# Kernel optimization log

Hardware: AMD Instinct MI355X
Metric: run time of the kernel (lower is better)

The kernel has to match this reference:

```python
import jax, jax.numpy as jnp
import numpy as np

B, A, D, F, O, NB = 64, 1024, 5, 256, 256, 6  # batch, max_atoms, max_degree, ishape, oshape, bond feat dim


def setup_inputs() -> dict:
    key = jax.random.key(0)
    k1, k2, k3, k4 = jax.random.split(key, 4)
    atoms = jax.random.normal(k1, (B, A, F), dtype=jnp.float32)
    bonds = jax.random.normal(k2, (B, A, D, NB), dtype=jnp.float32)
    # -1 marks missing neighbor (degree padding); valid indices in [0, A)
    edges = jax.random.randint(k3, (B, A, D), -1, A)
    # xavier-normal-ish init for the 6 degree-specific weights, stacked [6, F+NB, O]
    scale = (2.0 / (F + NB + O)) ** 0.5
    degW = jax.random.normal(k4, (6, F + NB, O), dtype=jnp.float32) * scale
    b = jnp.full((1, O), 0.01, dtype=jnp.float32)
    return {"atoms": atoms, "bonds": bonds, "edges": edges, "degW": degW, "b": b}


def reference(atoms, bonds, edges, degW, b):
    # atoms: [B, A, F]; bonds: [B, A, D, NB]; edges: [B, A, D] int (-1 = pad)
    degrees = (edges != -1).sum(-1, keepdims=True)  # [B, A, 1]
    # pad a zero row at index 0 so edge -1 -> 0 gathers the mask value 0
    padded = jnp.pad(atoms, ((0, 0), (1, 0), (0, 0)))  # [B, A+1, F]
    neigh = jax.vmap(lambda p, e: p[e])(padded, edges + 1)  # [B, A, D, F]
    summed_atom = atoms + neigh.sum(axis=2)  # include_self=True
    feats = jnp.concatenate([summed_atom, bonds.sum(axis=2)], axis=-1)  # [B, A, F+NB]
    out = jnp.zeros((atoms.shape[0], atoms.shape[1], degW.shape[-1]), atoms.dtype)
    for d in range(6):  # fixed small structural loop over degree buckets
        mask = (degrees == d).astype(atoms.dtype)  # [B, A, 1]
        out = out + jax.nn.sigmoid(feats @ degW[d] + b) * mask
    return out
```

## Files before the change

### kernel.cpp

```cpp
#include <hip/hip_runtime.h>
#include <cstdint>

#define BATCH  64
#define NATOMS 1024
#define DEG    5
#define FIN    256
#define OOUT   256
#define NBF    6
#define KDIM   262
#define NKT    9
#define MROWS  (BATCH * NATOMS)
#define MT     32
#define AS     296

#define FRAG_SHORTS (16 * NKT * 64 * 8)

typedef __attribute__((ext_vector_type(8))) short bf16x8;
typedef __attribute__((ext_vector_type(4))) float f32x4;

__device__ __forceinline__ unsigned short f2bf(float x) {
    unsigned u = __float_as_uint(x);
    u += 0x7fff + ((u >> 16) & 1);
    return (unsigned short)(u >> 16);
}
__device__ __forceinline__ float bf2f(unsigned short h) {
    return __uint_as_float(((unsigned)h) << 16);
}
__device__ __forceinline__ float sigmoidf_(float x) {
    return 1.f / (1.f + __expf(-x));
}

__global__ __launch_bounds__(256)
void convert_w_kernel(const float* __restrict__ degW, unsigned short* __restrict__ Wsw,
                      int all6)
{
    const int total = (all6 ? 6 : 1) * 16 * NKT * 64;
    const int idx = blockIdx.x * 256 + threadIdx.x;
    if (idx >= total) return;
    const int lane = idx & 63;
    int r = idx >> 6;
    const int t = r % NKT; r /= NKT;
    const int g = r & 15;
    const int d = r >> 4;
    const int srcd = all6 ? d : DEG;
    const int col  = g * 16 + (lane & 15);
    const int k0   = t * 32 + (lane >> 4) * 8;
    const float* __restrict__ W = degW + (size_t)srcd * KDIM * OOUT;
    unsigned short* dst = Wsw + (size_t)idx * 8;
    #pragma unroll
    for (int j = 0; j < 8; ++j) {
        const int k = k0 + j;
        dst[j] = f2bf((k < KDIM) ? W[(size_t)k * OOUT + col] : 0.f);
    }
}

__global__ __launch_bounds__(256, 4)
void nfp_fused_kernel(const float* __restrict__ atoms, const float* __restrict__ bonds,
                      const int* __restrict__ edges, const unsigned short* __restrict__ Wsw,
                      const float* __restrict__ degW, const float* __restrict__ bias,
                      float* __restrict__ out, int all6)
{
    __shared__ short Afeat[MT * AS];
    __shared__ int   edg[MT * DEG];
    __shared__ int   deg_lds[MT];
    __shared__ int   degmask;

    const int tid  = threadIdx.x;
    const int lane = tid & 63;
    const int wave = tid >> 6;

    const int bid   = blockIdx.x;
    const int xcd   = bid & 7;
    const int per   = bid >> 3;
    const int batch = (per >> 5) * 8 + xcd;
    const int blk   = per & 31;
    const int row0  = batch * NATOMS + blk * MT;

    if (tid == 0) degmask = 0;
    if (tid < MT * DEG) edg[tid] = edges[row0 * DEG + tid];
    __syncthreads();
    if (tid < MT) {
        int dc = 0;
        #pragma unroll
        for (int d = 0; d < DEG; ++d) dc += (edg[tid * DEG + d] != -1) ? 1 : 0;
        deg_lds[tid] = dc;
        atomicOr(&degmask, 1 << dc);
    }

    const float* __restrict__ abase = atoms + ((size_t)batch << 10) * FIN;
    const int selfrow = blk * MT;
    const int mw = wave * 8;

#define GATHER_CHUNK(MB, NR)                                                          \
    {                                                                                 \
        float4 self[NR]; float4 nv[NR][DEG]; int msk[NR];                             \
        _Pragma("unroll")                                                             \
        for (int r = 0; r < NR; ++r) {                                                \
            const int m = (MB) + r;                                                   \
            msk[r] = 0;                                                               \
            self[r] = *(const float4*)&abase[(size_t)(selfrow + m) * FIN + lane * 4]; \
            _Pragma("unroll")                                                         \
            for (int d = 0; d < DEG; ++d) {                                           \
                const int e = edg[m * DEG + d];                                       \
                msk[r] |= (e >= 0) ? (1 << d) : 0;                                    \
                const int ei = (e >= 0) ? e : 0;          \
                nv[r][d] = *(const float4*)&abase[(size_t)ei * FIN + lane * 4];       \
            }                                                                         \
        }                                                                             \
        _Pragma("unroll")                                                             \
        for (int r = 0; r < NR; ++r) {                                                \
            const int m = (MB) + r;                                                   \
            float4 v = self[r];                                                       \
            _Pragma("unroll")                                                         \
            for (int d = 0; d < DEG; ++d) {                                           \
                const float fl = ((msk[r] >> d) & 1) ? 1.f : 0.f;                     \
                v.x += fl * nv[r][d].x; v.y += fl * nv[r][d].y;                       \
                v.z += fl * nv[r][d].z; v.w += fl * nv[r][d].w;                       \
            }                                                                         \
            ushort4 us;                                                               \
            us.x = f2bf(v.x); us.y = f2bf(v.y); us.z = f2bf(v.z); us.w = f2bf(v.w);   \
            *(ushort4*)&Afeat[m * AS + lane * 4] = us;                                \
        }                                                                             \
    }

    GATHER_CHUNK(mw + 0, 3)
    GATHER_CHUNK(mw + 3, 3)
    GATHER_CHUNK(mw + 6, 2)
#undef GATHER_CHUNK

    {
        const int mz = mw + (lane >> 3), pz = lane & 7;
        ushort4 zz = {0, 0, 0, 0};
        *(ushort4*)&Afeat[mz * AS + FIN + pz * 4] = zz;
        if (lane < 48) {
            const int r  = lane / 6;
            const int kk = lane - r * 6;
            const int m  = mw + r;
            const float* __restrict__ bb = bonds + ((size_t)(row0 + m)) * (DEG * NBF) + kk;
            const float bv = bb[0] + bb[NBF] + bb[2 * NBF] + bb[3 * NBF] + bb[4 * NBF];
            Afeat[m * AS + FIN + kk] = f2bf(bv);
        }
    }

    const unsigned short* __restrict__ Wb5 =
        Wsw + (all6 ? (size_t)DEG * FRAG_SHORTS : (size_t)0);
    const int fr = lane & 15;
    const int q  = lane >> 4;
    const int wn = wave * 64;

    bf16x8 b0[4];
    #pragma unroll
    for (int j = 0; j < 4; ++j)
        b0[j] = *(const bf16x8*)&Wb5[((size_t)((wave * 4 + j) * NKT) * 64 + lane) * 8];

    __syncthreads();

    auto gemm_pass = [&](const unsigned short* __restrict__ Wb, bf16x8 (&bini)[4],
                         f32x4 (&a)[2][4]) {
        bf16x8 bcur[4], bnxt[4], acur[2], anxt[2];
        #pragma unroll
        for (int j = 0; j < 4; ++j) bcur[j] = bini[j];
        #pragma unroll
        for (int i = 0; i < 2; ++i)
            acur[i] = *(const bf16x8*)&Afeat[(i * 16 + fr) * AS + q * 8];
        #pragma unroll
        for (int t = 0; t < NKT; ++t) {
            if (t + 1 < NKT) {
                #pragma unroll
                for (int j = 0; j < 4; ++j)
                    bnxt[j] = *(const bf16x8*)&Wb[((size_t)((wave * 4 + j) * NKT + t + 1) * 64 + lane) * 8];
                #pragma unroll
                for (int i = 0; i < 2; ++i)
                    anxt[i] = *(const bf16x8*)&Afeat[(i * 16 + fr) * AS + (t + 1) * 32 + q * 8];
            }
            #pragma unroll
            for (int i = 0; i < 2; ++i)
                #pragma unroll
                for (int j = 0; j < 4; ++j)
                    a[i][j] = __builtin_amdgcn_mfma_f32_16x16x32_bf16(acur[i], bcur[j], a[i][j], 0, 0, 0);
            if (t + 1 < NKT) {
                #pragma unroll
                for (int j = 0; j < 4; ++j) bcur[j] = bnxt[j];
                #pragma unroll
                for (int i = 0; i < 2; ++i) acur[i] = anxt[i];
            }
        }
    };

    auto epilogue = [&](f32x4 (&a)[2][4], int want) {
        #pragma unroll
        for (int j = 0; j < 4; ++j) {
            const int gn = wn + j * 16 + fr;
            const float bj = bias[gn];
            #pragma unroll
            for (int i = 0; i < 2; ++i) {
                #pragma unroll
                for (int r = 0; r < 4; ++r) {
                    const int lm = i * 16 + q * 4 + r;
                    if (deg_lds[lm] == want)
                        __builtin_nontemporal_store(sigmoidf_(a[i][j][r] + bj),
                                                    &out[((size_t)row0 + lm) * OOUT + gn]);
                }
            }
        }
    };

    f32x4 acc[2][4];
    #pragma unroll
    for (int i = 0; i < 2; ++i)
        #pragma unroll
        for (int j = 0; j < 4; ++j)
            acc[i][j] = (f32x4){0.f, 0.f, 0.f, 0.f};

    gemm_pass(Wb5, b0, acc);
    epilogue(acc, DEG);

    int dmask = degmask & 0x1F;
    if (dmask == 0) return;

    if (all6) {
        while (dmask) {
            const int d = __ffs(dmask) - 1;
            dmask &= dmask - 1;
            const unsigned short* __restrict__ Wd = Wsw + (size_t)d * FRAG_SHORTS;
            bf16x8 bd[4];
            #pragma unroll
            for (int j = 0; j < 4; ++j)
                bd[j] = *(const bf16x8*)&Wd[((size_t)((wave * 4 + j) * NKT) * 64 + lane) * 8];
            f32x4 a2[2][4];
            #pragma unroll
            for (int i = 0; i < 2; ++i)
                #pragma unroll
                for (int j = 0; j < 4; ++j)
                    a2[i][j] = (f32x4){0.f, 0.f, 0.f, 0.f};
            gemm_pass(Wd, bd, a2);
            epilogue(a2, d);
        }
    } else {
        for (int m = 0; m < MT; ++m) {
            const int dg = deg_lds[m];
            if (dg == DEG) continue;
            const float* __restrict__ W = degW + (size_t)dg * KDIM * OOUT;
            float s0 = 0.f, s1 = 0.f, s2 = 0.f, s3 = 0.f;
            #pragma unroll 2
            for (int k = 0; k < 260; k += 4) {
                const float w0 = W[(size_t)(k + 0) * OOUT + tid];
                const float w1 = W[(size_t)(k + 1) * OOUT + tid];
                const float w2 = W[(size_t)(k + 2) * OOUT + tid];
                const float w3 = W[(size_t)(k + 3) * OOUT + tid];
                s0 += bf2f(Afeat[m * AS + k + 0]) * w0;
                s1 += bf2f(Afeat[m * AS + k + 1]) * w1;
                s2 += bf2f(Afeat[m * AS + k + 2]) * w2;
                s3 += bf2f(Afeat[m * AS + k + 3]) * w3;
            }
            s0 += bf2f(Afeat[m * AS + 260]) * W[(size_t)260 * OOUT + tid];
            s1 += bf2f(Afeat[m * AS + 261]) * W[(size_t)261 * OOUT + tid];
            const float x = ((s0 + s1) + (s2 + s3)) + bias[tid];
            out[((size_t)row0 + m) * OOUT + tid] = sigmoidf_(x);
        }
    }
}

#define FMT  32
#define FKT  32
#define FKPAD 288
__global__ __launch_bounds__(256, 2)
void nfp_conv_fallback(const float* __restrict__ atoms, const float* __restrict__ bonds,
                       const int* __restrict__ edges, const float* __restrict__ degW,
                       const float* __restrict__ bias, float* __restrict__ out)
{
    __shared__ float feats[FMT * FKPAD];
    __shared__ float wtile[FKT * OOUT];
    __shared__ int   edg[FMT * DEG];
    __shared__ int   deg_lds[FMT];
    __shared__ int   odd_list[FMT];
    __shared__ int   odd_cnt;
    __shared__ float b_lds[OOUT];

    const int tid = threadIdx.x, bid = blockIdx.x;
    const int batch = bid >> 5, a0 = (bid & 31) * FMT;
    const size_t atom_base = (size_t)batch * NATOMS;

    b_lds[tid] = bias[tid];
    if (tid == 0) odd_cnt = 0;
    if (tid < FMT * DEG) {
        const int m = tid / DEG, d = tid % DEG;
        edg[tid] = edges[(atom_base + a0 + m) * DEG + d];
    }
    __syncthreads();
    if (tid < FMT) {
        int dc = 0;
        #pragma unroll
        for (int d = 0; d < DEG; ++d) dc += (edg[tid * DEG + d] != -1) ? 1 : 0;
        deg_lds[tid] = dc;
        if (dc != DEG) { const int idx = atomicAdd(&odd_cnt, 1); odd_list[idx] = tid; }
    }
    __syncthreads();
    {
        const int f = tid;
        for (int m = 0; m < FMT; ++m) {
            float v = atoms[(atom_base + a0 + m) * FIN + f];
            #pragma unroll
            for (int d = 0; d < DEG; ++d) {
                const int e = edg[m * DEG + d];
                if (e >= 0) v += atoms[(atom_base + e) * FIN + f];
            }
            feats[m * FKPAD + f] = v;
        }
        #pragma unroll
        for (int t = 0; t < 4; ++t) {
            const int idx = t * 256 + tid;
            const int m = idx >> 5, kk = idx & 31;
            float v = 0.f;
            if (kk < NBF) {
                const size_t bb = (atom_base + a0 + m) * (size_t)(DEG * NBF);
                #pragma unroll
                for (int d = 0; d < DEG; ++d) v += bonds[bb + d * NBF + kk];
            }
            feats[m * FKPAD + FIN + kk] = v;
        }
    }
    const float* __restrict__ W5 = degW + (size_t)DEG * KDIM * OOUT;
    float acc[4][8];
    #pragma unroll
    for (int i = 0; i < 4; ++i)
        #pragma unroll
        for (int j = 0; j < 8; ++j) acc[i][j] = 0.f;
    const int tx = tid & 31, ty = tid >> 5;
    for (int kt = 0; kt < FKPAD; kt += FKT) {
        __syncthreads();
        #pragma unroll
        for (int t = 0; t < FKT; ++t) {
            const int k = kt + t;
            wtile[t * OOUT + tid] = (k < KDIM) ? W5[(size_t)k * OOUT + tid] : 0.f;
        }
        __syncthreads();
        #pragma unroll 4
        for (int r = 0; r < FKT; ++r) {
            float a_frag[4];
            #pragma unroll
            for (int i = 0; i < 4; ++i) a_frag[i] = feats[(ty * 4 + i) * FKPAD + kt + r];
            float w_frag[8];
            #pragma unroll
            for (int j = 0; j < 8; ++j) w_frag[j] = wtile[r * OOUT + tx + j * 32];
            #pragma unroll
            for (int i = 0; i < 4; ++i)
                #pragma unroll
                for (int j = 0; j < 8; ++j) acc[i][j] += a_frag[i] * w_frag[j];
        }
    }
    #pragma unroll
    for (int i = 0; i < 4; ++i) {
        const int m = ty * 4 + i;
        if (deg_lds[m] == DEG) {
            const size_t row = (atom_base + a0 + m) * (size_t)OOUT;
            #pragma unroll
            for (int j = 0; j < 8; ++j) {
                const int o = tx + j * 32;
                out[row + o] = sigmoidf_(acc[i][j] + b_lds[o]);
            }
        }
    }
    const int ocnt = odd_cnt;
    for (int i = 0; i < ocnt; ++i) {
        const int m = odd_list[i], d = deg_lds[m];
        const float* __restrict__ W = degW + (size_t)d * KDIM * OOUT;
        float a2 = 0.f;
        for (int k = 0; k < KDIM; ++k) a2 += feats[m * FKPAD + k] * W[(size_t)k * OOUT + tid];
        const size_t row = (atom_base + a0 + m) * (size_t)OOUT;
        out[row + tid] = sigmoidf_(a2 + b_lds[tid]);
    }
}

extern "C" void kernel_launch(void* const* d_in, const int* in_sizes, int n_in,
                              void* d_out, int out_size, void* d_ws, size_t ws_size,
                              hipStream_t stream) {
    const float* atoms = (const float*)d_in[0];
    const float* bonds = (const float*)d_in[1];
    const int*   edges = (const int*)d_in[2];
    const float* degW  = (const float*)d_in[3];
    const float* bias  = (const float*)d_in[4];
    float* out = (float*)d_out;

    const size_t WSW_ONE = (size_t)FRAG_SHORTS * 2;
    const size_t WSW_ALL = (size_t)6 * FRAG_SHORTS * 2;

    if (ws_size >= WSW_ALL) {
        unsigned short* Wsw = (unsigned short*)d_ws;
        convert_w_kernel<<<(6 * 16 * NKT * 64 + 255) / 256, 256, 0, stream>>>(degW, Wsw, 1);
        nfp_fused_kernel<<<MROWS / MT, 256, 0, stream>>>(
            atoms, bonds, edges, Wsw, degW, bias, out, 1);
    } else if (ws_size >= WSW_ONE) {
        unsigned short* Wsw = (unsigned short*)d_ws;
        convert_w_kernel<<<(16 * NKT * 64 + 255) / 256, 256, 0, stream>>>(degW, Wsw, 0);
        nfp_fused_kernel<<<MROWS / MT, 256, 0, stream>>>(
            atoms, bonds, edges, Wsw, degW, bias, out, 0);
    } else {
        nfp_conv_fallback<<<BATCH * (NATOMS / FMT), 256, 0, stream>>>(
            atoms, bonds, edges, degW, bias, out);
    }
}
```

Baseline: 196.5 us.

## Pre-convert atoms to fp16 so neighbor gathers read half the bytes

Adds a pre-pass, merged with the weight swizzle kernel, that writes an fp16 copy of the whole atoms tensor into workspace. The fused kernel then gathers neighbor rows from that copy while still loading self rows in fp32 with nontemporal loads. The goal is to halve the bytes moved by the five random-row gathers per atom. In exchange it adds a full extra read and write pass over atoms, lowers neighbor precision to fp16, and only runs when the workspace is large enough.

```diff
diff --git a/kernel.cpp b/kernel.cpp
--- a/kernel.cpp
+++ b/kernel.cpp
@@ -1,4 +1,5 @@
 #include <hip/hip_runtime.h>
+#include <hip/hip_fp16.h>
 #include <cstdint>
 
 #define BATCH  64
@@ -14,9 +15,11 @@
 #define AS     296
 
 #define FRAG_SHORTS (16 * NKT * 64 * 8)
+#define ATH_SHORTS  ((size_t)MROWS * FIN)
 
 typedef __attribute__((ext_vector_type(8))) short bf16x8;
 typedef __attribute__((ext_vector_type(4))) float f32x4;
+typedef __attribute__((ext_vector_type(4))) unsigned short u16x4;
 
 __device__ __forceinline__ unsigned short f2bf(float x) {
     unsigned u = __float_as_uint(x);
@@ -28,6 +31,50 @@
 }
 __device__ __forceinline__ float sigmoidf_(float x) {
     return 1.f / (1.f + __expf(-x));
+}
+__device__ __forceinline__ unsigned short f2h(float x) {
+    return __half_as_ushort(__float2half(x));
+}
+__device__ __forceinline__ float h2f(unsigned short u) {
+    return __half2float(__ushort_as_half(u));
+}
+
+__global__ __launch_bounds__(256)
+void convert_pre_kernel(const float* __restrict__ degW, unsigned short* __restrict__ Wsw,
+                        const float* __restrict__ atoms, unsigned short* __restrict__ atomsH,
+                        int nWblk)
+{
+    if (blockIdx.x < (unsigned)nWblk) {
+        const int idx = blockIdx.x * 256 + threadIdx.x;
+        if (idx >= 6 * 16 * NKT * 64) return;
+        const int lane = idx & 63;
+        int r = idx >> 6;
+        const int t = r % NKT; r /= NKT;
+        const int g = r & 15;
+        const int d = r >> 4;
+        const int col  = g * 16 + (lane & 15);
+        const int k0   = t * 32 + (lane >> 4) * 8;
+        const float* __restrict__ W = degW + (size_t)d * KDIM * OOUT;
+        unsigned short* dst = Wsw + (size_t)idx * 8;
+        #pragma unroll
+        for (int j = 0; j < 8; ++j) {
+            const int k = k0 + j;
+            dst[j] = f2bf((k < KDIM) ? W[(size_t)k * OOUT + col] : 0.f);
+        }
+    } else {
+        const int nblk = gridDim.x - nWblk;
+        size_t i = (size_t)(blockIdx.x - nWblk) * 256 + threadIdx.x;
+        const size_t stride = (size_t)nblk * 256;
+        const size_t total = ATH_SHORTS / 4;
+        const f32x4* __restrict__ src = (const f32x4*)atoms;
+        u16x4* __restrict__ dst = (u16x4*)atomsH;
+        for (; i < total; i += stride) {
+            f32x4 v = __builtin_nontemporal_load(&src[i]);
+            u16x4 h;
+            h.x = f2h(v.x); h.y = f2h(v.y); h.z = f2h(v.z); h.w = f2h(v.w);
+            __builtin_nontemporal_store(h, &dst[i]);
+        }
+    }
 }
 
 __global__ __launch_bounds__(256)
@@ -54,12 +101,16 @@
     }
 }
 
+template <int MODE>
 __global__ __launch_bounds__(256, 4)
-void nfp_fused_kernel(const float* __restrict__ atoms, const float* __restrict__ bonds,
-                      const int* __restrict__ edges, const unsigned short* __restrict__ Wsw,
-                      const float* __restrict__ degW, const float* __restrict__ bias,
-                      float* __restrict__ out, int all6)
+void nfp_fused_kernel(const float* __restrict__ atoms, const unsigned short* __restrict__ atomsH,
+                      const float* __restrict__ bonds, const int* __restrict__ edges,
+                      const unsigned short* __restrict__ Wsw, const float* __restrict__ degW,
+                      const float* __restrict__ bias, float* __restrict__ out)
 {
+    constexpr bool FP16N = (MODE == 2);
+    constexpr bool ALL6  = (MODE >= 1);
+
     __shared__ short Afeat[MT * AS];
     __shared__ int   edg[MT * DEG];
     __shared__ int   deg_lds[MT];
@@ -88,38 +139,50 @@
     }
 
     const float* __restrict__ abase = atoms + ((size_t)batch << 10) * FIN;
+    const unsigned short* __restrict__ hbase =
+        FP16N ? atomsH + ((size_t)batch << 10) * FIN : atomsH;
     const int selfrow = blk * MT;
     const int mw = wave * 8;
 
 #define GATHER_CHUNK(MB, NR)                                                          \
     {                                                                                 \
-        float4 self[NR]; float4 nv[NR][DEG]; int msk[NR];                             \
+        f32x4 self[NR]; int msk[NR];                                                  \
+        u16x4 nh[NR][DEG]; f32x4 nv[NR][DEG];                                         \
         _Pragma("unroll")                                                             \
         for (int r = 0; r < NR; ++r) {                                                \
             const int m = (MB) + r;                                                   \
             msk[r] = 0;                                                               \
-            self[r] = *(const float4*)&abase[(size_t)(selfrow + m) * FIN + lane * 4]; \
+            self[r] = __builtin_nontemporal_load(                                     \
+                (const f32x4*)&abase[(size_t)(selfrow + m) * FIN + lane * 4]);        \
             _Pragma("unroll")                                                         \
             for (int d = 0; d < DEG; ++d) {                                           \
                 const int e = edg[m * DEG + d];                                       \
                 msk[r] |= (e >= 0) ? (1 << d) : 0;                                    \
                 const int ei = (e >= 0) ? e : 0;          \
-                nv[r][d] = *(const float4*)&abase[(size_t)ei * FIN + lane * 4];       \
+                if constexpr (FP16N)                                                  \
+                    nh[r][d] = *(const u16x4*)&hbase[(size_t)ei * FIN + lane * 4];    \
+                else                                                                  \
+                    nv[r][d] = *(const f32x4*)&abase[(size_t)ei * FIN + lane * 4];    \
             }                                                                         \
         }                                                                             \
         _Pragma("unroll")                                                             \
         for (int r = 0; r < NR; ++r) {                                                \
             const int m = (MB) + r;                                                   \
-            float4 v = self[r];                                                       \
+            f32x4 v = self[r];                                                        \
             _Pragma("unroll")                                                         \
             for (int d = 0; d < DEG; ++d) {                                           \
                 const float fl = ((msk[r] >> d) & 1) ? 1.f : 0.f;                     \
-                v.x += fl * nv[r][d].x; v.y += fl * nv[r][d].y;                       \
-                v.z += fl * nv[r][d].z; v.w += fl * nv[r][d].w;                       \
+                if constexpr (FP16N) {                                                \
+                    v.x += fl * h2f(nh[r][d].x); v.y += fl * h2f(nh[r][d].y);         \
+                    v.z += fl * h2f(nh[r][d].z); v.w += fl * h2f(nh[r][d].w);         \
+                } else {                                                              \
+                    v.x += fl * nv[r][d].x; v.y += fl * nv[r][d].y;                   \
+                    v.z += fl * nv[r][d].z; v.w += fl * nv[r][d].w;                   \
+                }                                                                     \
             }                                                                         \
-            ushort4 us;                                                               \
+            u16x4 us;                                                                 \
             us.x = f2bf(v.x); us.y = f2bf(v.y); us.z = f2bf(v.z); us.w = f2bf(v.w);   \
-            *(ushort4*)&Afeat[m * AS + lane * 4] = us;                                \
+            *(u16x4*)&Afeat[m * AS + lane * 4] = us;                                  \
         }                                                                             \
     }
 
@@ -130,8 +193,8 @@
 
     {
         const int mz = mw + (lane >> 3), pz = lane & 7;
-        ushort4 zz = {0, 0, 0, 0};
-        *(ushort4*)&Afeat[mz * AS + FIN + pz * 4] = zz;
+        u16x4 zz = {0, 0, 0, 0};
+        *(u16x4*)&Afeat[mz * AS + FIN + pz * 4] = zz;
         if (lane < 48) {
             const int r  = lane / 6;
             const int kk = lane - r * 6;
@@ -143,7 +206,7 @@
     }
 
     const unsigned short* __restrict__ Wb5 =
-        Wsw + (all6 ? (size_t)DEG * FRAG_SHORTS : (size_t)0);
+        Wsw + (ALL6 ? (size_t)DEG * FRAG_SHORTS : (size_t)0);
     const int fr = lane & 15;
     const int q  = lane >> 4;
     const int wn = wave * 64;
@@ -218,7 +281,7 @@
     int dmask = degmask & 0x1F;
     if (dmask == 0) return;
 
-    if (all6) {
+    if constexpr (ALL6) {
         while (dmask) {
             const int d = __ffs(dmask) - 1;
             dmask &= dmask - 1;
@@ -384,17 +447,25 @@
 
     const size_t WSW_ONE = (size_t)FRAG_SHORTS * 2;
     const size_t WSW_ALL = (size_t)6 * FRAG_SHORTS * 2;
-
-    if (ws_size >= WSW_ALL) {
+    const size_t ATH_B   = ATH_SHORTS * 2;
+
+    if (ws_size >= WSW_ALL + ATH_B) {
+        unsigned short* Wsw    = (unsigned short*)d_ws;
+        unsigned short* atomsH = (unsigned short*)((char*)d_ws + WSW_ALL);
+        const int nWblk = (6 * 16 * NKT * 64 + 255) / 256;
+        convert_pre_kernel<<<nWblk + 2048, 256, 0, stream>>>(degW, Wsw, atoms, atomsH, nWblk);
+        nfp_fused_kernel<2><<<MROWS / MT, 256, 0, stream>>>(
+            atoms, atomsH, bonds, edges, Wsw, degW, bias, out);
+    } else if (ws_size >= WSW_ALL) {
         unsigned short* Wsw = (unsigned short*)d_ws;
         convert_w_kernel<<<(6 * 16 * NKT * 64 + 255) / 256, 256, 0, stream>>>(degW, Wsw, 1);
-        nfp_fused_kernel<<<MROWS / MT, 256, 0, stream>>>(
-            atoms, bonds, edges, Wsw, degW, bias, out, 1);
+        nfp_fused_kernel<1><<<MROWS / MT, 256, 0, stream>>>(
+            atoms, nullptr, bonds, edges, Wsw, degW, bias, out);
     } else if (ws_size >= WSW_ONE) {
         unsigned short* Wsw = (unsigned short*)d_ws;
         convert_w_kernel<<<(16 * NKT * 64 + 255) / 256, 256, 0, stream>>>(degW, Wsw, 0);
-        nfp_fused_kernel<<<MROWS / MT, 256, 0, stream>>>(
-            atoms, bonds, edges, Wsw, degW, bias, out, 0);
+        nfp_fused_kernel<0><<<MROWS / MT, 256, 0, stream>>>(
+            atoms, nullptr, bonds, edges, Wsw, degW, bias, out);
     } else {
         nfp_conv_fallback<<<BATCH * (NATOMS / FMT), 256, 0, stream>>>(
             atoms, bonds, edges, degW, bias, out);
```

After: 214.9 us. 1.09x slower.
